# Kernel optimization log

Measured on AMD Instinct MI355X. Metric: run time of the kernel, lower is better.

The kernel has to match this reference:

```python
import jax, jax.numpy as jnp
import numpy as np
import math

BS, S, D, H, DFF, L = 32, 512, 512, 8, 2048, 2
DK = D // H
K_INDEX = 5
NEG = -1e32


def _xavier(key, shape):
    fan_out, fan_in = shape[-2], shape[-1]
    lim = math.sqrt(6.0 / (fan_in + fan_out))
    return jax.random.uniform(key, shape, minval=-lim, maxval=lim, dtype=jnp.float32)


def _cosine_pe():
    pos = np.arange(S, dtype=np.float32)[:, None]
    div = np.exp(np.arange(0, D, 2, dtype=np.float32) * -(math.log(10000.0) / D))
    pe = np.zeros((S, D), dtype=np.float32)
    pe[:, 0::2] = np.sin(pos * div)
    pe[:, 1::2] = np.cos(pos * div)
    return jnp.asarray(pe)[None]  # [1,S,D]


def setup_inputs() -> dict:
    key = jax.random.key(0)
    ks = jax.random.split(key, 8)
    return {
        'q_embed_data': jax.random.normal(ks[0], (BS, S, D), jnp.float32),
        'qa_embed_data': jax.random.normal(ks[1], (BS, S, D), jnp.float32),
        'pe': _cosine_pe(),
        'Wk': _xavier(ks[2], (L, D, D)), 'bk': jnp.zeros((L, D)),
        'Wv': _xavier(ks[3], (L, D, D)), 'bv': jnp.zeros((L, D)),
        'Wo': _xavier(ks[4], (L, D, D)), 'bo': jnp.zeros((L, D)),
        'W1': _xavier(ks[5], (L, DFF, D)), 'b1': jnp.zeros((L, DFF)),
        'W2': _xavier(ks[6], (L, D, DFF)), 'b2': jnp.zeros((L, D)),
        'ln1w': jnp.ones((L, D)), 'ln1b': jnp.zeros((L, D)),
        'ln2w': jnp.ones((L, D)), 'ln2b': jnp.zeros((L, D)),
    }


def _ln(x, w, b):
    m = jnp.mean(x, axis=-1, keepdims=True)
    v = jnp.mean((x - m) ** 2, axis=-1, keepdims=True)
    return (x - m) / jnp.sqrt(v + 1e-5) * w + b


def _forward(q_embed_data, qa_embed_data, pe, Wk, bk, Wv, bv, Wo, bo,
             W1, b1, W2, b2, ln1w, ln1b, ln2w, ln2b):
    x = q_embed_data + pe[:, :S]
    y = qa_embed_data + pe[:, :S]
    # src_mask = (triu(ones, k=0) == 0): only strictly-lower positions allowed (row 0 fully masked)
    causal = jnp.tril(jnp.ones((S, S), bool), k=-1)
    attn_weights = None
    for l in range(L):
        # kq_same: q uses k_linear
        q = (x @ Wk[l].T + bk[l]).reshape(BS, S, H, DK).transpose(0, 2, 1, 3)
        k = q  # identical projection of identical input (key=query=x)
        v = (y @ Wv[l].T + bv[l]).reshape(BS, S, H, DK).transpose(0, 2, 1, 3)
        scores = jnp.einsum('bhqd,bhkd->bhqk', q, k) / math.sqrt(DK)
        scores = jnp.where(causal, scores, NEG)
        scores = jax.nn.softmax(scores, axis=-1)
        # sparseattn: for rows >= K_INDEX keep only entries >= k-th largest, re-softmax
        sb = scores[:, :, K_INDEX:, :]
        thr = jax.lax.top_k(sb, K_INDEX)[0][..., -1:]  # k-th largest per row
        sb = jnp.where(sb - thr >= 0, sb, NEG)
        scores = jnp.concatenate([scores[:, :, :K_INDEX, :], sb], axis=2)
        scores = jax.nn.softmax(scores, axis=-1)
        attn_weights = scores  # before_dropout_scores (before zero_pad)
        scores = scores.at[:, :, 0, :].set(0.0)  # zero_pad row 0
        out = jnp.einsum('bhqk,bhkd->bhqd', scores, v)
        out = out.transpose(0, 2, 1, 3).reshape(BS, S, D) @ Wo[l].T + bo[l]
        x = _ln(x + out, ln1w[l], ln1b[l])
        ff = jax.nn.relu(x @ W1[l].T + b1[l]) @ W2[l].T + b2[l]
        x = _ln(x + ff, ln2w[l], ln2b[l])
    return x, attn_weights


def reference(q_embed_data, qa_embed_data, pe, Wk, bk, Wv, bv, Wo, bo,
              W1, b1, W2, b2, ln1w, ln1b, ln2w, ln2b):
    return _forward(q_embed_data, qa_embed_data, pe, Wk, bk, Wv, bv, Wo, bo,
                    W1, b1, W2, b2, ln1w, ln1b, ln2w, ln2b)
```

## Files before the change

kernel.cpp:

```cpp
#include <hip/hip_runtime.h>
#include <hip/hip_bf16.h>
#include <math.h>

#define BSZ 32
#define SEQ 512
#define DIM 512
#define NH 8
#define DKH 64
#define DFFN 2048
#define NL 2
#define KIDX 5
#define NEGV -1e32f

typedef float f32x4 __attribute__((ext_vector_type(4)));
typedef short bf16x8 __attribute__((ext_vector_type(8)));
typedef unsigned short ushort_t;

__device__ __forceinline__ float wmaxf(float v) {
    #pragma unroll
    for (int m = 32; m > 0; m >>= 1) v = fmaxf(v, __shfl_xor(v, m));
    return v;
}
__device__ __forceinline__ float wsumf(float v) {
    #pragma unroll
    for (int m = 32; m > 0; m >>= 1) v += __shfl_xor(v, m);
    return v;
}
__device__ __forceinline__ int wsumi(int v) {
    #pragma unroll
    for (int m = 32; m > 0; m >>= 1) v += __shfl_xor(v, m);
    return v;
}

__device__ __forceinline__ unsigned int bf16_rne(float x) {
    unsigned int u = __float_as_uint(x);
    return (u + 0x7fffu + ((u >> 16) & 1u)) >> 16;
}
__device__ __forceinline__ void split3_8(const float* xs, unsigned int* hh,
                                         unsigned int* hm, unsigned int* hl) {
    #pragma unroll
    for (int e = 0; e < 8; e++) {
        float x = xs[e];
        unsigned int h0 = bf16_rne(x);
        float r1 = x - __uint_as_float(h0 << 16);
        unsigned int h1 = bf16_rne(r1);
        float r2 = r1 - __uint_as_float(h1 << 16);
        hh[e] = h0; hm[e] = h1; hl[e] = bf16_rne(r2);
    }
}
__device__ __forceinline__ uint4 pack8(const unsigned int* h) {
    return make_uint4(h[0] | (h[1] << 16), h[2] | (h[3] << 16),
                      h[4] | (h[5] << 16), h[6] | (h[7] << 16));
}

__device__ __forceinline__ f32x4 mfma_bf16(bf16x8 a, bf16x8 b, f32x4 c) {
    return __builtin_amdgcn_mfma_f32_16x16x32_bf16(a, b, c, 0, 0, 0);
}

__global__ void add_pe_old(const float4* __restrict__ q, const float4* __restrict__ qa,
                           const float4* __restrict__ pe, float4* __restrict__ x,
                           float4* __restrict__ y, int n4) {
    int i = blockIdx.x * 256 + threadIdx.x;
    if (i >= n4) return;
    int pi = i & (SEQ * DIM / 4 - 1);
    float4 p = pe[pi];
    float4 a = q[i], b = qa[i];
    x[i] = make_float4(a.x + p.x, a.y + p.y, a.z + p.z, a.w + p.w);
    y[i] = make_float4(b.x + p.x, b.y + p.y, b.z + p.z, b.w + p.w);
}

__global__ void add_pe_new(const float* __restrict__ q, const float* __restrict__ qa,
                           const float* __restrict__ pe, float* __restrict__ x,
                           ushort_t* __restrict__ ypl, size_t yelems, int n8) {
    int i = blockIdx.x * 256 + threadIdx.x;
    if (i >= n8) return;
    size_t base = (size_t)i * 8;
    size_t pb = base & (size_t)(SEQ * DIM - 1);
    float4 a0 = *(const float4*)(q + base), a1 = *(const float4*)(q + base + 4);
    float4 b0 = *(const float4*)(qa + base), b1 = *(const float4*)(qa + base + 4);
    float4 p0 = *(const float4*)(pe + pb), p1 = *(const float4*)(pe + pb + 4);
    float4 x0 = make_float4(a0.x + p0.x, a0.y + p0.y, a0.z + p0.z, a0.w + p0.w);
    float4 x1 = make_float4(a1.x + p1.x, a1.y + p1.y, a1.z + p1.z, a1.w + p1.w);
    *(float4*)(x + base) = x0;
    *(float4*)(x + base + 4) = x1;
    float ys[8] = {b0.x + p0.x, b0.y + p0.y, b0.z + p0.z, b0.w + p0.w,
                   b1.x + p1.x, b1.y + p1.y, b1.z + p1.z, b1.w + p1.w};
    unsigned int hh[8], hm[8], hl[8];
    split3_8(ys, hh, hm, hl);
    *(uint4*)(ypl + base) = pack8(hh);
    *(uint4*)(ypl + yelems + base) = pack8(hm);
    *(uint4*)(ypl + 2 * yelems + base) = pack8(hl);
}

__global__ void split3w(const float* __restrict__ W, ushort_t* __restrict__ out,
                        size_t elems, int n8) {
    int i = blockIdx.x * 256 + threadIdx.x;
    if (i >= n8) return;
    size_t base = (size_t)i * 8;
    float4 a0 = *(const float4*)(W + base), a1 = *(const float4*)(W + base + 4);
    float xs[8] = {a0.x, a0.y, a0.z, a0.w, a1.x, a1.y, a1.z, a1.w};
    unsigned int hh[8], hm[8], hl[8];
    split3_8(xs, hh, hm, hl);
    *(uint4*)(out + base) = pack8(hh);
    *(uint4*)(out + elems + base) = pack8(hm);
    *(uint4*)(out + 2 * elems + base) = pack8(hl);
}

template <int RELU>
__global__ __launch_bounds__(256)
void gemm_bt(const float* __restrict__ A, const float* __restrict__ B,
             const float* __restrict__ bias, float* __restrict__ C,
             int M, int N, int K) {
    __shared__ float As[16][132];
    __shared__ float Bs[16][132];
    const int tid = threadIdx.x;
    const int tx = tid & 15, ty = tid >> 4;
    const int m0 = blockIdx.y * 128, n0 = blockIdx.x * 128;
    float acc[8][8] = {};
    for (int k0 = 0; k0 < K; k0 += 16) {
        #pragma unroll
        for (int s = tid; s < 512; s += 256) {
            int r = s >> 2, c4 = s & 3;
            float4 va = *(const float4*)(A + (size_t)(m0 + r) * K + k0 + c4 * 4);
            As[c4 * 4 + 0][r] = va.x; As[c4 * 4 + 1][r] = va.y;
            As[c4 * 4 + 2][r] = va.z; As[c4 * 4 + 3][r] = va.w;
            float4 vb = *(const float4*)(B + (size_t)(n0 + r) * K + k0 + c4 * 4);
            Bs[c4 * 4 + 0][r] = vb.x; Bs[c4 * 4 + 1][r] = vb.y;
            Bs[c4 * 4 + 2][r] = vb.z; Bs[c4 * 4 + 3][r] = vb.w;
        }
        __syncthreads();
        #pragma unroll
        for (int kk = 0; kk < 16; kk++) {
            float a[8], b[8];
            *(float4*)&a[0] = *(const float4*)&As[kk][ty * 8];
            *(float4*)&a[4] = *(const float4*)&As[kk][ty * 8 + 4];
            *(float4*)&b[0] = *(const float4*)&Bs[kk][tx * 8];
            *(float4*)&b[4] = *(const float4*)&Bs[kk][tx * 8 + 4];
            #pragma unroll
            for (int i = 0; i < 8; i++)
                #pragma unroll
                for (int j = 0; j < 8; j++)
                    acc[i][j] = fmaf(a[i], b[j], acc[i][j]);
        }
        __syncthreads();
    }
    float bv[8];
    *(float4*)&bv[0] = *(const float4*)(bias + n0 + tx * 8);
    *(float4*)&bv[4] = *(const float4*)(bias + n0 + tx * 8 + 4);
    #pragma unroll
    for (int i = 0; i < 8; i++) {
        float out[8];
        #pragma unroll
        for (int j = 0; j < 8; j++) {
            float v = acc[i][j] + bv[j];
            if (RELU) v = fmaxf(v, 0.f);
            out[j] = v;
        }
        float* cp = C + (size_t)(m0 + ty * 8 + i) * N + n0 + tx * 8;
        *(float4*)cp = *(float4*)&out[0];
        *(float4*)(cp + 4) = *(float4*)&out[4];
    }
}

__global__ __launch_bounds__(256)
void scores128_kernel(const float* __restrict__ q, float* __restrict__ pbuf) {
    const int bh = blockIdx.y, b = bh >> 3, h = bh & 7;
    const int x = blockIdx.x;
    const int it = (x >= 6) ? 3 : (x >= 3) ? 2 : (x >= 1) ? 1 : 0;
    const int jt = x - it * (it + 1) / 2;
    const int m0 = it * 128, n0 = jt * 128;
    __shared__ float Qi[64][132];
    __shared__ float Qj[64][132];
    const float* qbase = q + (size_t)b * SEQ * DIM + h * DKH;
    const int tid = threadIdx.x;
    for (int s = tid; s < 2048; s += 256) {
        int row = (s & 15) | ((s >> 8) << 4);
        int c4 = (s >> 4) & 15;
        float4 vi = *(const float4*)(qbase + (size_t)(m0 + row) * DIM + c4 * 4);
        Qi[c4 * 4 + 0][row] = vi.x; Qi[c4 * 4 + 1][row] = vi.y;
        Qi[c4 * 4 + 2][row] = vi.z; Qi[c4 * 4 + 3][row] = vi.w;
        float4 vj = *(const float4*)(qbase + (size_t)(n0 + row) * DIM + c4 * 4);
        Qj[c4 * 4 + 0][row] = vj.x; Qj[c4 * 4 + 1][row] = vj.y;
        Qj[c4 * 4 + 2][row] = vj.z; Qj[c4 * 4 + 3][row] = vj.w;
    }
    __syncthreads();
    const int tx = tid & 15, ty = tid >> 4;
    float acc[8][8] = {};
    #pragma unroll 4
    for (int d = 0; d < 64; d++) {
        float a[8], bb[8];
        *(float4*)&a[0] = *(const float4*)&Qi[d][ty * 8];
        *(float4*)&a[4] = *(const float4*)&Qi[d][ty * 8 + 4];
        *(float4*)&bb[0] = *(const float4*)&Qj[d][tx * 8];
        *(float4*)&bb[4] = *(const float4*)&Qj[d][tx * 8 + 4];
        #pragma unroll
        for (int i = 0; i < 8; i++)
            #pragma unroll
            for (int j = 0; j < 8; j++)
                acc[i][j] = fmaf(a[i], bb[j], acc[i][j]);
    }
    float* prow = pbuf + ((size_t)bh * SEQ + m0) * SEQ + n0;
    #pragma unroll
    for (int i = 0; i < 8; i++) {
        int gi = m0 + ty * 8 + i;
        #pragma unroll
        for (int jq = 0; jq < 2; jq++) {
            float o[4];
            #pragma unroll
            for (int j = 0; j < 4; j++) {
                int gj = n0 + tx * 8 + jq * 4 + j;
                o[j] = (gj < gi) ? acc[i][jq * 4 + j] * 0.125f : NEGV;
            }
            *(float4*)(prow + (size_t)(ty * 8 + i) * SEQ + tx * 8 + jq * 4) = *(float4*)o;
        }
    }
}

template <int RELU, int OUTP>
__global__ __launch_bounds__(256) void gemm3p(
    const ushort_t* __restrict__ Apl, size_t Aelems, int lda,
    const ushort_t* __restrict__ Bpl, size_t Belems, int ldb,
    const float* __restrict__ bias,
    float* __restrict__ C, ushort_t* __restrict__ Cpl, size_t Celems,
    int ldc, int K) {
    __shared__ uint4 lds[3072];
    const int tid = threadIdx.x, lane = tid & 63, wid = tid >> 6;
    const int wm = wid >> 1, wn = wid & 1;
    const int m0 = blockIdx.y * 128, n0 = blockIdx.x * 128;
    const int lrow = lane & 15, lkof = (lane >> 4) * 8;
    f32x4 acc[4][4] = {};
    for (int k0 = 0; k0 < K; k0 += 32) {
        #pragma unroll
        for (int t = 0; t < 12; t++) {
            const ushort_t* src;
            int dstoff;
            if (t < 6) {
                int cc = wid + t * 4;
                int p = cc >> 3, fi = cc & 7;
                src = Apl + (size_t)p * Aelems + (size_t)(m0 + fi * 16 + lrow) * lda + k0 + lkof;
                dstoff = p * 512 + fi * 64;
            } else {
                int cc = wid + (t - 6) * 4;
                int p = cc >> 3, fi = cc & 7;
                src = Bpl + (size_t)p * Belems + (size_t)(n0 + fi * 16 + lrow) * ldb + k0 + lkof;
                dstoff = 1536 + p * 512 + fi * 64;
            }
            lds[dstoff + lane] = *(const uint4*)src;
        }
        __syncthreads();
        const bf16x8* ldsb = (const bf16x8*)lds;
        bf16x8 afr[4][3];
        #pragma unroll
        for (int fm = 0; fm < 4; fm++)
            #pragma unroll
            for (int p = 0; p < 3; p++)
                afr[fm][p] = ldsb[p * 512 + (wm * 4 + fm) * 64 + lane];
        #pragma unroll
        for (int fn = 0; fn < 4; fn++) {
            bf16x8 b0 = ldsb[1536 + 0 * 512 + (wn * 4 + fn) * 64 + lane];
            bf16x8 b1 = ldsb[1536 + 1 * 512 + (wn * 4 + fn) * 64 + lane];
            bf16x8 b2 = ldsb[1536 + 2 * 512 + (wn * 4 + fn) * 64 + lane];
            #pragma unroll
            for (int fm = 0; fm < 4; fm++) {
                f32x4 t = acc[fm][fn];
                t = mfma_bf16(afr[fm][0], b0, t);
                t = mfma_bf16(afr[fm][1], b0, t);
                t = mfma_bf16(afr[fm][2], b0, t);
                t = mfma_bf16(afr[fm][0], b1, t);
                t = mfma_bf16(afr[fm][1], b1, t);
                t = mfma_bf16(afr[fm][0], b2, t);
                acc[fm][fn] = t;
            }
        }
        __syncthreads();
    }
    #pragma unroll
    for (int fm = 0; fm < 4; fm++) {
        int row0 = m0 + (wm * 4 + fm) * 16 + (lane >> 4) * 4;
        #pragma unroll
        for (int fn = 0; fn < 4; fn++) {
            int col = n0 + (wn * 4 + fn) * 16 + (lane & 15);
            float bv = bias[col];
            f32x4 a = acc[fm][fn];
            #pragma unroll
            for (int r = 0; r < 4; r++) {
                int row = row0 + r;
                float val = a[r] + bv;
                if (RELU) val = fmaxf(val, 0.f);
                if constexpr (OUTP == 0) {
                    C[(size_t)row * ldc + col] = val;
                } else {
                    unsigned int h0 = bf16_rne(val);
                    float r1 = val - __uint_as_float(h0 << 16);
                    unsigned int h1 = bf16_rne(r1);
                    float r2 = r1 - __uint_as_float(h1 << 16);
                    unsigned int h2 = bf16_rne(r2);
                    size_t o = (size_t)row * ldc + col;
                    Cpl[o] = (ushort_t)h0;
                    Cpl[Celems + o] = (ushort_t)h1;
                    Cpl[2 * Celems + o] = (ushort_t)h2;
                }
            }
        }
    }
}

template <int MODE, int TN>
__global__ __launch_bounds__(256) void mm6(const float* __restrict__ Aall,
                                           const float* __restrict__ Ball,
                                           float* __restrict__ Call,
                                           const float* __restrict__ bias,
                                           int lda, int ldb, int ldc, int K) {
    constexpr int BFR = TN / 16;
    constexpr int MFR = (TN == 128) ? 4 : 2;
    constexpr int BBASE = 3 * 8 * 64;
    __shared__ uint4 lds[3 * 8 * 64 + 3 * BFR * 64];

    const int tid = threadIdx.x, lane = tid & 63, wid = tid >> 6;
    const int wm = (TN == 128) ? (wid >> 1) : wid;
    const int wn = (TN == 128) ? (wid & 1) : 0;

    const float* A;
    const float* B;
    float* C;
    int m0, n0, kmax;
    if constexpr (MODE <= 1) {
        m0 = blockIdx.y * 128;
        n0 = blockIdx.x * 128;
        A = Aall; B = Ball; C = Call;
        kmax = K;
    } else {
        const int bh = blockIdx.y, b = bh >> 3, h = bh & 7, rb = blockIdx.x;
        m0 = rb * 128; n0 = 0;
        A = Aall + (size_t)bh * SEQ * SEQ;
        B = Ball + (size_t)bh * DKH * SEQ;
        C = Call + ((size_t)b * SEQ) * DIM + h * DKH;
        kmax = rb ? (rb + 1) * 128 : SEQ;
    }

    f32x4 acc[MFR][4] = {};

    for (int k0 = 0; k0 < kmax; k0 += 32) {
        for (int c = tid; c < (8 + BFR) * 64; c += 256) {
            int fi = c >> 6, lc = c & 63;
            const float* src = (fi < 8)
                ? A + (size_t)(m0 + fi * 16 + (lc & 15)) * lda + k0 + (lc >> 4) * 8
                : B + (size_t)(n0 + (fi - 8) * 16 + (lc & 15)) * ldb + k0 + (lc >> 4) * 8;
            float4 x0 = *(const float4*)src;
            float4 x1 = *(const float4*)(src + 4);
            float xs[8] = {x0.x, x0.y, x0.z, x0.w, x1.x, x1.y, x1.z, x1.w};
            unsigned int hh[8], hm[8], hl[8];
            split3_8(xs, hh, hm, hl);
            int base = (fi < 8) ? fi * 64 + lc : BBASE + (fi - 8) * 64 + lc;
            int fstride = (fi < 8) ? 8 * 64 : BFR * 64;
            lds[base + 0 * fstride] = pack8(hh);
            lds[base + 1 * fstride] = pack8(hm);
            lds[base + 2 * fstride] = pack8(hl);
        }
        __syncthreads();

        const bf16x8* ldsb = (const bf16x8*)lds;
        bf16x8 afr[MFR][3];
        #pragma unroll
        for (int fm = 0; fm < MFR; fm++)
            #pragma unroll
            for (int p = 0; p < 3; p++)
                afr[fm][p] = ldsb[p * 512 + (wm * MFR + fm) * 64 + lane];
        #pragma unroll
        for (int fn = 0; fn < 4; fn++) {
            bf16x8 b0 = ldsb[BBASE + 0 * (BFR * 64) + (wn * 4 + fn) * 64 + lane];
            bf16x8 b1 = ldsb[BBASE + 1 * (BFR * 64) + (wn * 4 + fn) * 64 + lane];
            bf16x8 b2 = ldsb[BBASE + 2 * (BFR * 64) + (wn * 4 + fn) * 64 + lane];
            #pragma unroll
            for (int fm = 0; fm < MFR; fm++) {
                f32x4 t = acc[fm][fn];
                t = mfma_bf16(afr[fm][0], b0, t);
                t = mfma_bf16(afr[fm][1], b0, t);
                t = mfma_bf16(afr[fm][2], b0, t);
                t = mfma_bf16(afr[fm][0], b1, t);
                t = mfma_bf16(afr[fm][1], b1, t);
                t = mfma_bf16(afr[fm][0], b2, t);
                acc[fm][fn] = t;
            }
        }
        __syncthreads();
    }

    #pragma unroll
    for (int fm = 0; fm < MFR; fm++) {
        int row0 = m0 + (wm * MFR + fm) * 16 + (lane >> 4) * 4;
        #pragma unroll
        for (int fn = 0; fn < 4; fn++) {
            int col = n0 + (wn * 4 + fn) * 16 + (lane & 15);
            float bv = 0.f;
            if constexpr (MODE <= 1) bv = bias[col];
            f32x4 a = acc[fm][fn];
            #pragma unroll
            for (int r = 0; r < 4; r++) {
                int row = row0 + r;
                float val;
                if constexpr (MODE == 0) val = a[r] + bv;
                else if constexpr (MODE == 1) val = fmaxf(a[r] + bv, 0.f);
                else val = (row == 0) ? 0.f : a[r];
                C[(size_t)row * ldc + col] = val;
            }
        }
    }
}

__global__ __launch_bounds__(256) void mm6av_pl(const float* __restrict__ pbuf,
                                                const float* __restrict__ vt,
                                                ushort_t* __restrict__ Opl, size_t Oelems) {
    constexpr int BFR = 4, MFR = 2, BBASE = 3 * 8 * 64;
    __shared__ uint4 lds[3 * 8 * 64 + 3 * BFR * 64];
    const int tid = threadIdx.x, lane = tid & 63, wid = tid >> 6;
    const int bh = blockIdx.y, b = bh >> 3, h = bh & 7, rb = blockIdx.x;
    const int m0 = rb * 128;
    const float* A = pbuf + (size_t)bh * SEQ * SEQ;
    const float* B = vt + (size_t)bh * DKH * SEQ;
    const int kmax = rb ? (rb + 1) * 128 : SEQ;

    f32x4 acc[MFR][4] = {};
    for (int k0 = 0; k0 < kmax; k0 += 32) {
        for (int c = tid; c < (8 + BFR) * 64; c += 256) {
            int fi = c >> 6, lc = c & 63;
            const float* src = (fi < 8)
                ? A + (size_t)(m0 + fi * 16 + (lc & 15)) * SEQ + k0 + (lc >> 4) * 8
                : B + (size_t)((fi - 8) * 16 + (lc & 15)) * SEQ + k0 + (lc >> 4) * 8;
            float4 x0 = *(const float4*)src;
            float4 x1 = *(const float4*)(src + 4);
            float xs[8] = {x0.x, x0.y, x0.z, x0.w, x1.x, x1.y, x1.z, x1.w};
            unsigned int hh[8], hm[8], hl[8];
            split3_8(xs, hh, hm, hl);
            int base = (fi < 8) ? fi * 64 + lc : BBASE + (fi - 8) * 64 + lc;
            int fstride = (fi < 8) ? 8 * 64 : BFR * 64;
            lds[base + 0 * fstride] = pack8(hh);
            lds[base + 1 * fstride] = pack8(hm);
            lds[base + 2 * fstride] = pack8(hl);
        }
        __syncthreads();
        const bf16x8* ldsb = (const bf16x8*)lds;
        bf16x8 afr[MFR][3];
        #pragma unroll
        for (int fm = 0; fm < MFR; fm++)
            #pragma unroll
            for (int p = 0; p < 3; p++)
                afr[fm][p] = ldsb[p * 512 + (wid * MFR + fm) * 64 + lane];
        #pragma unroll
        for (int fn = 0; fn < 4; fn++) {
            bf16x8 b0 = ldsb[BBASE + 0 * (BFR * 64) + fn * 64 + lane];
            bf16x8 b1 = ldsb[BBASE + 1 * (BFR * 64) + fn * 64 + lane];
            bf16x8 b2 = ldsb[BBASE + 2 * (BFR * 64) + fn * 64 + lane];
            #pragma unroll
            for (int fm = 0; fm < MFR; fm++) {
                f32x4 t = acc[fm][fn];
                t = mfma_bf16(afr[fm][0], b0, t);
                t = mfma_bf16(afr[fm][1], b0, t);
                t = mfma_bf16(afr[fm][2], b0, t);
                t = mfma_bf16(afr[fm][0], b1, t);
                t = mfma_bf16(afr[fm][1], b1, t);
                t = mfma_bf16(afr[fm][0], b2, t);
                acc[fm][fn] = t;
            }
        }
        __syncthreads();
    }
    #pragma unroll
    for (int fm = 0; fm < MFR; fm++) {
        int row0 = m0 + (wid * MFR + fm) * 16 + (lane >> 4) * 4;
        #pragma unroll
        for (int fn = 0; fn < 4; fn++) {
            int col = fn * 16 + (lane & 15);
            f32x4 a = acc[fm][fn];
            #pragma unroll
            for (int r = 0; r < 4; r++) {
                int row = row0 + r;
                float val = (row == 0) ? 0.f : a[r];
                unsigned int h0 = bf16_rne(val);
                float r1 = val - __uint_as_float(h0 << 16);
                unsigned int h1 = bf16_rne(r1);
                float r2 = r1 - __uint_as_float(h1 << 16);
                unsigned int h2 = bf16_rne(r2);
                size_t o = ((size_t)b * SEQ + row) * DIM + h * DKH + col;
                Opl[o] = (ushort_t)h0;
                Opl[Oelems + o] = (ushort_t)h1;
                Opl[2 * Oelems + o] = (ushort_t)h2;
            }
        }
    }
}

__global__ __launch_bounds__(256) void transpose_v_kernel(const float* __restrict__ v,
                                                          float* __restrict__ vt) {
    const int bh = blockIdx.y, jt = blockIdx.x;
    const int b = bh >> 3, h = bh & 7;
    __shared__ float L[64][65];
    const int tid = threadIdx.x;
    for (int s = tid; s < 1024; s += 256) {
        int jj = s >> 4, d4 = s & 15;
        float4 x = *(const float4*)(v + ((size_t)(b * SEQ) + jt * 64 + jj) * DIM + h * DKH + d4 * 4);
        L[jj][d4 * 4 + 0] = x.x; L[jj][d4 * 4 + 1] = x.y;
        L[jj][d4 * 4 + 2] = x.z; L[jj][d4 * 4 + 3] = x.w;
    }
    __syncthreads();
    int d = tid >> 2, jq = tid & 3;
    float* dst = vt + ((size_t)bh * DKH + d) * SEQ + jt * 64 + jq * 16;
    #pragma unroll
    for (int c4 = 0; c4 < 4; c4++) {
        float4 o = make_float4(L[jq * 16 + c4 * 4 + 0][d], L[jq * 16 + c4 * 4 + 1][d],
                               L[jq * 16 + c4 * 4 + 2][d], L[jq * 16 + c4 * 4 + 3][d]);
        *(float4*)(dst + c4 * 4) = o;
    }
}

__global__ __launch_bounds__(64)
void softmax_topk_kernel(float* __restrict__ pbuf) {
    const int i = blockIdx.x;
    const size_t row = (size_t)blockIdx.y * SEQ + i;
    const int lane = threadIdx.x;
    float* p = pbuf + row * SEQ;
    float v[8];
    {
        int j0 = lane * 4;
        if (j0 < i) {
            float4 x0 = *(const float4*)(p + j0);
            v[0] = (j0 + 0 < i) ? x0.x : NEGV;
            v[1] = (j0 + 1 < i) ? x0.y : NEGV;
            v[2] = (j0 + 2 < i) ? x0.z : NEGV;
            v[3] = (j0 + 3 < i) ? x0.w : NEGV;
        } else { v[0] = v[1] = v[2] = v[3] = NEGV; }
        int j1 = 256 + j0;
        if (j1 < i) {
            float4 x1 = *(const float4*)(p + j1);
            v[4] = (j1 + 0 < i) ? x1.x : NEGV;
            v[5] = (j1 + 1 < i) ? x1.y : NEGV;
            v[6] = (j1 + 2 < i) ? x1.z : NEGV;
            v[7] = (j1 + 3 < i) ? x1.w : NEGV;
        } else { v[4] = v[5] = v[6] = v[7] = NEGV; }
    }
    float lm = v[0];
    #pragma unroll
    for (int e = 1; e < 8; e++) lm = fmaxf(lm, v[e]);
    float m1 = wmaxf(lm);
    float ls = 0.f;
    #pragma unroll
    for (int e = 0; e < 8; e++) { v[e] = expf(v[e] - m1); ls += v[e]; }
    float Z = wsumf(ls);
    #pragma unroll
    for (int e = 0; e < 8; e++) v[e] = v[e] / Z;
    float thr = -INFINITY;
    if (i >= KIDX) {
        int remaining = KIDX;
        float cut = INFINITY;
        #pragma unroll 1
        for (int iter = 0; iter < KIDX; iter++) {
            float l2 = -INFINITY;
            #pragma unroll
            for (int e = 0; e < 8; e++) if (v[e] < cut) l2 = fmaxf(l2, v[e]);
            float m2 = wmaxf(l2);
            int lc = 0;
            #pragma unroll
            for (int e = 0; e < 8; e++) if (v[e] == m2) lc++;
            int c = wsumi(lc);
            if (c >= remaining) { thr = m2; break; }
            remaining -= c; cut = m2;
        }
    }
    float lpm = v[0];
    #pragma unroll
    for (int e = 1; e < 8; e++) lpm = fmaxf(lpm, v[e]);
    float pm = wmaxf(lpm);
    float t[8];
    float ls2 = 0.f;
    #pragma unroll
    for (int e = 0; e < 8; e++) {
        bool keep = (i >= KIDX) ? (v[e] >= thr) : true;
        t[e] = keep ? expf(v[e] - pm) : 0.f;
        ls2 += t[e];
    }
    float Z2 = wsumf(ls2);
    #pragma unroll
    for (int e = 0; e < 8; e++) t[e] = t[e] / Z2;
    *(float4*)(p + lane * 4) = make_float4(t[0], t[1], t[2], t[3]);
    *(float4*)(p + 256 + lane * 4) = make_float4(t[4], t[5], t[6], t[7]);
}

template <int EMIT>
__global__ __launch_bounds__(64)
void add_ln_kernel(const float* __restrict__ x, const float* __restrict__ t,
                   const float* __restrict__ w, const float* __restrict__ b,
                   float* __restrict__ dst, ushort_t* __restrict__ dpl, size_t delems) {
    const size_t row = blockIdx.x;
    const int lane = threadIdx.x;
    const float* xr = x + row * DIM;
    const float* tr = t + row * DIM;
    float v[8];
    {
        float4 a0 = *(const float4*)(xr + lane * 4);
        float4 t0 = *(const float4*)(tr + lane * 4);
        float4 a1 = *(const float4*)(xr + 256 + lane * 4);
        float4 t1 = *(const float4*)(tr + 256 + lane * 4);
        v[0] = a0.x + t0.x; v[1] = a0.y + t0.y; v[2] = a0.z + t0.z; v[3] = a0.w + t0.w;
        v[4] = a1.x + t1.x; v[5] = a1.y + t1.y; v[6] = a1.z + t1.z; v[7] = a1.w + t1.w;
    }
    float ls = 0.f;
    #pragma unroll
    for (int e = 0; e < 8; e++) ls += v[e];
    float mean = wsumf(ls) / (float)DIM;
    float ld = 0.f;
    #pragma unroll
    for (int e = 0; e < 8; e++) { float d = v[e] - mean; ld += d * d; }
    float var = wsumf(ld) / (float)DIM;
    float den = sqrtf(var + 1e-5f);
    float wv[8], bv[8];
    *(float4*)&wv[0] = *(const float4*)(w + lane * 4);
    *(float4*)&wv[4] = *(const float4*)(w + 256 + lane * 4);
    *(float4*)&bv[0] = *(const float4*)(b + lane * 4);
    *(float4*)&bv[4] = *(const float4*)(b + 256 + lane * 4);
    float o[8];
    #pragma unroll
    for (int e = 0; e < 8; e++) o[e] = (v[e] - mean) / den * wv[e] + bv[e];
    float* dr = dst + row * DIM;
    *(float4*)(dr + lane * 4) = make_float4(o[0], o[1], o[2], o[3]);
    *(float4*)(dr + 256 + lane * 4) = make_float4(o[4], o[5], o[6], o[7]);
    if constexpr (EMIT) {
        unsigned int hh[8], hm[8], hl[8];
        split3_8(o, hh, hm, hl);
        size_t base0 = row * DIM + lane * 4;
        size_t base1 = base0 + 256;
        #pragma unroll
        for (int p = 0; p < 3; p++) {
            const unsigned int* hp = (p == 0) ? hh : (p == 1) ? hm : hl;
            *(uint2*)(dpl + p * delems + base0) =
                make_uint2(hp[0] | (hp[1] << 16), hp[2] | (hp[3] << 16));
            *(uint2*)(dpl + p * delems + base1) =
                make_uint2(hp[4] | (hp[5] << 16), hp[6] | (hp[7] << 16));
        }
    }
}

extern "C" void kernel_launch(void* const* d_in, const int* in_sizes, int n_in,
                              void* d_out, int out_size, void* d_ws, size_t ws_size,
                              hipStream_t stream) {
    const float* q_embed = (const float*)d_in[0];
    const float* qa_embed = (const float*)d_in[1];
    const float* pe = (const float*)d_in[2];
    const float* Wk = (const float*)d_in[3];
    const float* bk = (const float*)d_in[4];
    const float* Wv = (const float*)d_in[5];
    const float* bv = (const float*)d_in[6];
    const float* Wo = (const float*)d_in[7];
    const float* bo = (const float*)d_in[8];
    const float* W1 = (const float*)d_in[9];
    const float* b1 = (const float*)d_in[10];
    const float* W2 = (const float*)d_in[11];
    const float* b2 = (const float*)d_in[12];
    const float* ln1w = (const float*)d_in[13];
    const float* ln1b = (const float*)d_in[14];
    const float* ln2w = (const float*)d_in[15];
    const float* ln2b = (const float*)d_in[16];

    float* outx = (float*)d_out;
    const size_t NE = (size_t)BSZ * SEQ * DIM;
    float* pbuf = outx + NE;
    float* ws = (float*)d_ws;
    const int M = BSZ * SEQ;

    const size_t need_new = 13 * NE * sizeof(float);
    if (ws_size >= need_new) {
        float* xbuf = ws;
        float* qbuf = ws + NE;
        float* vbuf = ws + 2 * NE;
        ushort_t* y_pl = (ushort_t*)(ws + 3 * NE);
        ushort_t* x_pl = (ushort_t*)(ws + 4 * NE + NE / 2);
        ushort_t* w_pl = (ushort_t*)(ws + 6 * NE);
        float* vt = ws + 7 * NE;
        ushort_t* o_pl = (ushort_t*)(ws + 8 * NE);
        ushort_t* h1_pl = (ushort_t*)(ws + 7 * NE);

        const size_t WVE = (size_t)DIM * DIM;
        const size_t W1E = (size_t)DFFN * DIM;
        const size_t LW = 3 * (WVE + WVE + W1E + W1E);

        for (int l = 0; l < NL; l++) {
            ushort_t* base = w_pl + (size_t)l * LW;
            split3w<<<(int)(WVE / 8 + 255) / 256, 256, 0, stream>>>(
                Wv + (size_t)l * WVE, base, WVE, (int)(WVE / 8));
            split3w<<<(int)(WVE / 8 + 255) / 256, 256, 0, stream>>>(
                Wo + (size_t)l * WVE, base + 3 * WVE, WVE, (int)(WVE / 8));
            split3w<<<(int)(W1E / 8 + 255) / 256, 256, 0, stream>>>(
                W1 + (size_t)l * W1E, base + 6 * WVE, W1E, (int)(W1E / 8));
            split3w<<<(int)(W1E / 8 + 255) / 256, 256, 0, stream>>>(
                W2 + (size_t)l * W1E, base + 6 * WVE + 3 * W1E, W1E, (int)(W1E / 8));
        }

        add_pe_new<<<(int)(NE / 8 + 255) / 256, 256, 0, stream>>>(
            q_embed, qa_embed, pe, xbuf, y_pl, NE, (int)(NE / 8));

        for (int l = 0; l < NL; l++) {
            ushort_t* wb = w_pl + (size_t)l * LW;
            ushort_t* Wv_pl = wb;
            ushort_t* Wo_pl = wb + 3 * WVE;
            ushort_t* W1_pl = wb + 6 * WVE;
            ushort_t* W2_pl = wb + 6 * WVE + 3 * W1E;

            gemm_bt<0><<<dim3(DIM / 128, M / 128), 256, 0, stream>>>(
                xbuf, Wk + (size_t)l * WVE, bk + (size_t)l * DIM, qbuf, M, DIM, DIM);
            gemm3p<0, 0><<<dim3(DIM / 128, M / 128), 256, 0, stream>>>(
                y_pl, NE, DIM, Wv_pl, WVE, DIM, bv + (size_t)l * DIM,
                vbuf, nullptr, 0, DIM, DIM);
            transpose_v_kernel<<<dim3(8, BSZ * NH), 256, 0, stream>>>(vbuf, vt);
            scores128_kernel<<<dim3(10, BSZ * NH), 256, 0, stream>>>(qbuf, pbuf);
            softmax_topk_kernel<<<dim3(SEQ, BSZ * NH), 64, 0, stream>>>(pbuf);
            mm6av_pl<<<dim3(4, BSZ * NH), 256, 0, stream>>>(pbuf, vt, o_pl, NE);
            gemm3p<0, 0><<<dim3(DIM / 128, M / 128), 256, 0, stream>>>(
                o_pl, NE, DIM, Wo_pl, WVE, DIM, bo + (size_t)l * DIM,
                qbuf, nullptr, 0, DIM, DIM);
            add_ln_kernel<1><<<M, 64, 0, stream>>>(
                xbuf, qbuf, ln1w + (size_t)l * DIM, ln1b + (size_t)l * DIM,
                xbuf, x_pl, NE);
            gemm3p<1, 1><<<dim3(DFFN / 128, M / 128), 256, 0, stream>>>(
                x_pl, NE, DIM, W1_pl, W1E, DIM, b1 + (size_t)l * DFFN,
                nullptr, h1_pl, (size_t)M * DFFN, DFFN, DIM);
            gemm3p<0, 0><<<dim3(DIM / 128, M / 128), 256, 0, stream>>>(
                h1_pl, (size_t)M * DFFN, DFFN, W2_pl, W1E, DFFN, b2 + (size_t)l * DIM,
                vbuf, nullptr, 0, DIM, DFFN);
            float* dst = (l == NL - 1) ? outx : xbuf;
            add_ln_kernel<0><<<M, 64, 0, stream>>>(
                xbuf, vbuf, ln2w + (size_t)l * DIM, ln2b + (size_t)l * DIM,
                dst, nullptr, 0);
        }
    } else {
        float* xbuf = ws;
        float* ybuf = ws + NE;
        float* qbuf = ws + 2 * NE;
        float* vbuf = ws + 3 * NE;
        float* obuf = ws + 4 * NE;
        float* vtbuf = ws + 5 * NE;
        float* h1buf = ws + 5 * NE;

        {
            int n4 = (int)(NE / 4);
            add_pe_old<<<(n4 + 255) / 256, 256, 0, stream>>>(
                (const float4*)q_embed, (const float4*)qa_embed, (const float4*)pe,
                (float4*)xbuf, (float4*)ybuf, n4);
        }
        for (int l = 0; l < NL; l++) {
            const float* Wk_l = Wk + (size_t)l * DIM * DIM;
            const float* Wv_l = Wv + (size_t)l * DIM * DIM;
            const float* Wo_l = Wo + (size_t)l * DIM * DIM;
            const float* W1_l = W1 + (size_t)l * DFFN * DIM;
            const float* W2_l = W2 + (size_t)l * DIM * DFFN;

            gemm_bt<0><<<dim3(DIM / 128, M / 128), 256, 0, stream>>>(
                xbuf, Wk_l, bk + (size_t)l * DIM, qbuf, M, DIM, DIM);
            mm6<0, 128><<<dim3(DIM / 128, M / 128), 256, 0, stream>>>(
                ybuf, Wv_l, vbuf, bv + (size_t)l * DIM, DIM, DIM, DIM, DIM);
            transpose_v_kernel<<<dim3(8, BSZ * NH), 256, 0, stream>>>(vbuf, vtbuf);
            scores128_kernel<<<dim3(10, BSZ * NH), 256, 0, stream>>>(qbuf, pbuf);
            softmax_topk_kernel<<<dim3(SEQ, BSZ * NH), 64, 0, stream>>>(pbuf);
            mm6<3, 64><<<dim3(4, BSZ * NH), 256, 0, stream>>>(
                pbuf, vtbuf, obuf, nullptr, SEQ, SEQ, DIM, SEQ);
            mm6<0, 128><<<dim3(DIM / 128, M / 128), 256, 0, stream>>>(
                obuf, Wo_l, qbuf, bo + (size_t)l * DIM, DIM, DIM, DIM, DIM);
            add_ln_kernel<0><<<M, 64, 0, stream>>>(
                xbuf, qbuf, ln1w + (size_t)l * DIM, ln1b + (size_t)l * DIM,
                xbuf, nullptr, 0);
            mm6<1, 128><<<dim3(DFFN / 128, M / 128), 256, 0, stream>>>(
                xbuf, W1_l, h1buf, b1 + (size_t)l * DFFN, DIM, DIM, DFFN, DIM);
            mm6<0, 128><<<dim3(DIM / 128, M / 128), 256, 0, stream>>>(
                h1buf, W2_l, vbuf, b2 + (size_t)l * DIM, DFFN, DFFN, DIM, DFFN);
            float* dst = (l == NL - 1) ? outx : xbuf;
            add_ln_kernel<0><<<M, 64, 0, stream>>>(
                xbuf, vbuf, ln2w + (size_t)l * DIM, ln2b + (size_t)l * DIM,
                dst, nullptr, 0);
        }
    }
}
```

Baseline: 2.194 ms.

## Use two-plane bf16 split in last layer and direct global-to-LDS loads

Templates the bf16-split GEMMs on the number of planes and runs the second layer with two planes (3 MFMAs per tile step instead of 6), skipping the third residual plane both in inputs and in emitted outputs. It also replaces register-staged global loads in gemm3p with global_load_lds direct-to-LDS transfers. Lower emulated precision in the last layer cuts MFMA and memory work but loosens accuracy relative to the fp32 reference.

```diff
diff --git a/kernel.cpp b/kernel.cpp
--- a/kernel.cpp
+++ b/kernel.cpp
@@ -15,6 +15,12 @@
 typedef float f32x4 __attribute__((ext_vector_type(4)));
 typedef short bf16x8 __attribute__((ext_vector_type(8)));
 typedef unsigned short ushort_t;
+typedef __attribute__((address_space(1))) void gvoid;
+typedef __attribute__((address_space(3))) void lvoid;
+
+__device__ __forceinline__ void gload_lds16(const void* g, void* l) {
+    __builtin_amdgcn_global_load_lds((gvoid*)(uintptr_t)g, (lvoid*)l, 16, 0, 0);
+}
 
 __device__ __forceinline__ float wmaxf(float v) {
     #pragma unroll
@@ -216,14 +222,15 @@
     }
 }
 
-template <int RELU, int OUTP>
+template <int RELU, int OUTP, int NP>
 __global__ __launch_bounds__(256) void gemm3p(
     const ushort_t* __restrict__ Apl, size_t Aelems, int lda,
     const ushort_t* __restrict__ Bpl, size_t Belems, int ldb,
     const float* __restrict__ bias,
     float* __restrict__ C, ushort_t* __restrict__ Cpl, size_t Celems,
     int ldc, int K) {
-    __shared__ uint4 lds[3072];
+    constexpr int BB = NP * 512;
+    __shared__ uint4 lds[2 * NP * 512];
     const int tid = threadIdx.x, lane = tid & 63, wid = tid >> 6;
     const int wm = wid >> 1, wn = wid & 1;
     const int m0 = blockIdx.y * 128, n0 = blockIdx.x * 128;
@@ -231,44 +238,46 @@
     f32x4 acc[4][4] = {};
     for (int k0 = 0; k0 < K; k0 += 32) {
         #pragma unroll
-        for (int t = 0; t < 12; t++) {
-            const ushort_t* src;
-            int dstoff;
-            if (t < 6) {
-                int cc = wid + t * 4;
-                int p = cc >> 3, fi = cc & 7;
-                src = Apl + (size_t)p * Aelems + (size_t)(m0 + fi * 16 + lrow) * lda + k0 + lkof;
-                dstoff = p * 512 + fi * 64;
-            } else {
-                int cc = wid + (t - 6) * 4;
-                int p = cc >> 3, fi = cc & 7;
-                src = Bpl + (size_t)p * Belems + (size_t)(n0 + fi * 16 + lrow) * ldb + k0 + lkof;
-                dstoff = 1536 + p * 512 + fi * 64;
-            }
-            lds[dstoff + lane] = *(const uint4*)src;
+        for (int t = 0; t < 4 * NP; t++) {
+            int cc = wid + t * 4;
+            bool isB = cc >= 8 * NP;
+            int c2 = isB ? (cc - 8 * NP) : cc;
+            int p = c2 >> 3, fi = c2 & 7;
+            const ushort_t* pb = isB ? (Bpl + (size_t)p * Belems) : (Apl + (size_t)p * Aelems);
+            int ld = isB ? ldb : lda;
+            int r0 = isB ? n0 : m0;
+            const ushort_t* src = pb + (size_t)(r0 + fi * 16 + lrow) * ld + k0 + lkof;
+            gload_lds16(src, &lds[(isB ? BB : 0) + p * 512 + fi * 64]);
         }
         __syncthreads();
         const bf16x8* ldsb = (const bf16x8*)lds;
-        bf16x8 afr[4][3];
+        bf16x8 afr[4][NP];
         #pragma unroll
         for (int fm = 0; fm < 4; fm++)
             #pragma unroll
-            for (int p = 0; p < 3; p++)
+            for (int p = 0; p < NP; p++)
                 afr[fm][p] = ldsb[p * 512 + (wm * 4 + fm) * 64 + lane];
         #pragma unroll
         for (int fn = 0; fn < 4; fn++) {
-            bf16x8 b0 = ldsb[1536 + 0 * 512 + (wn * 4 + fn) * 64 + lane];
-            bf16x8 b1 = ldsb[1536 + 1 * 512 + (wn * 4 + fn) * 64 + lane];
-            bf16x8 b2 = ldsb[1536 + 2 * 512 + (wn * 4 + fn) * 64 + lane];
+            bf16x8 b0 = ldsb[BB + 0 * 512 + (wn * 4 + fn) * 64 + lane];
+            bf16x8 b1 = ldsb[BB + 1 * 512 + (wn * 4 + fn) * 64 + lane];
+            bf16x8 b2;
+            if constexpr (NP == 3) b2 = ldsb[BB + 2 * 512 + (wn * 4 + fn) * 64 + lane];
             #pragma unroll
             for (int fm = 0; fm < 4; fm++) {
                 f32x4 t = acc[fm][fn];
-                t = mfma_bf16(afr[fm][0], b0, t);
-                t = mfma_bf16(afr[fm][1], b0, t);
-                t = mfma_bf16(afr[fm][2], b0, t);
-                t = mfma_bf16(afr[fm][0], b1, t);
-                t = mfma_bf16(afr[fm][1], b1, t);
-                t = mfma_bf16(afr[fm][0], b2, t);
+                if constexpr (NP == 3) {
+                    t = mfma_bf16(afr[fm][0], b0, t);
+                    t = mfma_bf16(afr[fm][1], b0, t);
+                    t = mfma_bf16(afr[fm][2], b0, t);
+                    t = mfma_bf16(afr[fm][0], b1, t);
+                    t = mfma_bf16(afr[fm][1], b1, t);
+                    t = mfma_bf16(afr[fm][0], b2, t);
+                } else {
+                    t = mfma_bf16(afr[fm][0], b0, t);
+                    t = mfma_bf16(afr[fm][1], b0, t);
+                    t = mfma_bf16(afr[fm][0], b1, t);
+                }
                 acc[fm][fn] = t;
             }
         }
@@ -293,12 +302,13 @@
                     unsigned int h0 = bf16_rne(val);
                     float r1 = val - __uint_as_float(h0 << 16);
                     unsigned int h1 = bf16_rne(r1);
-                    float r2 = r1 - __uint_as_float(h1 << 16);
-                    unsigned int h2 = bf16_rne(r2);
                     size_t o = (size_t)row * ldc + col;
                     Cpl[o] = (ushort_t)h0;
                     Cpl[Celems + o] = (ushort_t)h1;
-                    Cpl[2 * Celems + o] = (ushort_t)h2;
+                    if constexpr (NP == 3) {
+                        float r2 = r1 - __uint_as_float(h1 << 16);
+                        Cpl[2 * Celems + o] = (ushort_t)bf16_rne(r2);
+                    }
                 }
             }
         }
@@ -408,11 +418,12 @@
     }
 }
 
+template <int NP>
 __global__ __launch_bounds__(256) void mm6av_pl(const float* __restrict__ pbuf,
                                                 const float* __restrict__ vt,
                                                 ushort_t* __restrict__ Opl, size_t Oelems) {
-    constexpr int BFR = 4, MFR = 2, BBASE = 3 * 8 * 64;
-    __shared__ uint4 lds[3 * 8 * 64 + 3 * BFR * 64];
+    constexpr int BBASE = NP * 512;
+    __shared__ uint4 lds[NP * 512 + NP * 256];
     const int tid = threadIdx.x, lane = tid & 63, wid = tid >> 6;
     const int bh = blockIdx.y, b = bh >> 3, h = bh & 7, rb = blockIdx.x;
     const int m0 = rb * 128;
@@ -420,9 +431,9 @@
     const float* B = vt + (size_t)bh * DKH * SEQ;
     const int kmax = rb ? (rb + 1) * 128 : SEQ;
 
-    f32x4 acc[MFR][4] = {};
+    f32x4 acc[2][4] = {};
     for (int k0 = 0; k0 < kmax; k0 += 32) {
-        for (int c = tid; c < (8 + BFR) * 64; c += 256) {
+        for (int c = tid; c < 12 * 64; c += 256) {
             int fi = c >> 6, lc = c & 63;
             const float* src = (fi < 8)
                 ? A + (size_t)(m0 + fi * 16 + (lc & 15)) * SEQ + k0 + (lc >> 4) * 8
@@ -432,42 +443,50 @@
             float xs[8] = {x0.x, x0.y, x0.z, x0.w, x1.x, x1.y, x1.z, x1.w};
             unsigned int hh[8], hm[8], hl[8];
             split3_8(xs, hh, hm, hl);
-            int base = (fi < 8) ? fi * 64 + lc : BBASE + (fi - 8) * 64 + lc;
-            int fstride = (fi < 8) ? 8 * 64 : BFR * 64;
-            lds[base + 0 * fstride] = pack8(hh);
-            lds[base + 1 * fstride] = pack8(hm);
-            lds[base + 2 * fstride] = pack8(hl);
+            int base, fstride;
+            if (fi < 8) { base = fi * 64 + lc; fstride = 512; }
+            else { base = BBASE + (fi - 8) * 64 + lc; fstride = 256; }
+            lds[base] = pack8(hh);
+            lds[base + fstride] = pack8(hm);
+            if (NP == 3) lds[base + 2 * fstride] = pack8(hl);
         }
         __syncthreads();
         const bf16x8* ldsb = (const bf16x8*)lds;
-        bf16x8 afr[MFR][3];
-        #pragma unroll
-        for (int fm = 0; fm < MFR; fm++)
-            #pragma unroll
-            for (int p = 0; p < 3; p++)
-                afr[fm][p] = ldsb[p * 512 + (wid * MFR + fm) * 64 + lane];
+        bf16x8 afr[2][NP];
+        #pragma unroll
+        for (int fm = 0; fm < 2; fm++)
+            #pragma unroll
+            for (int p = 0; p < NP; p++)
+                afr[fm][p] = ldsb[p * 512 + (wid * 2 + fm) * 64 + lane];
         #pragma unroll
         for (int fn = 0; fn < 4; fn++) {
-            bf16x8 b0 = ldsb[BBASE + 0 * (BFR * 64) + fn * 64 + lane];
-            bf16x8 b1 = ldsb[BBASE + 1 * (BFR * 64) + fn * 64 + lane];
-            bf16x8 b2 = ldsb[BBASE + 2 * (BFR * 64) + fn * 64 + lane];
-            #pragma unroll
-            for (int fm = 0; fm < MFR; fm++) {
+            bf16x8 b0 = ldsb[BBASE + 0 * 256 + fn * 64 + lane];
+            bf16x8 b1 = ldsb[BBASE + 1 * 256 + fn * 64 + lane];
+            bf16x8 b2;
+            if constexpr (NP == 3) b2 = ldsb[BBASE + 2 * 256 + fn * 64 + lane];
+            #pragma unroll
+            for (int fm = 0; fm < 2; fm++) {
                 f32x4 t = acc[fm][fn];
-                t = mfma_bf16(afr[fm][0], b0, t);
-                t = mfma_bf16(afr[fm][1], b0, t);
-                t = mfma_bf16(afr[fm][2], b0, t);
-                t = mfma_bf16(afr[fm][0], b1, t);
-                t = mfma_bf16(afr[fm][1], b1, t);
-                t = mfma_bf16(afr[fm][0], b2, t);
+                if constexpr (NP == 3) {
+                    t = mfma_bf16(afr[fm][0], b0, t);
+                    t = mfma_bf16(afr[fm][1], b0, t);
+                    t = mfma_bf16(afr[fm][2], b0, t);
+                    t = mfma_bf16(afr[fm][0], b1, t);
+                    t = mfma_bf16(afr[fm][1], b1, t);
+                    t = mfma_bf16(afr[fm][0], b2, t);
+                } else {
+                    t = mfma_bf16(afr[fm][0], b0, t);
+                    t = mfma_bf16(afr[fm][1], b0, t);
+                    t = mfma_bf16(afr[fm][0], b1, t);
+                }
                 acc[fm][fn] = t;
             }
         }
         __syncthreads();
     }
     #pragma unroll
-    for (int fm = 0; fm < MFR; fm++) {
-        int row0 = m0 + (wid * MFR + fm) * 16 + (lane >> 4) * 4;
+    for (int fm = 0; fm < 2; fm++) {
+        int row0 = m0 + (wid * 2 + fm) * 16 + (lane >> 4) * 4;
         #pragma unroll
         for (int fn = 0; fn < 4; fn++) {
             int col = fn * 16 + (lane & 15);
@@ -479,12 +498,13 @@
                 unsigned int h0 = bf16_rne(val);
                 float r1 = val - __uint_as_float(h0 << 16);
                 unsigned int h1 = bf16_rne(r1);
-                float r2 = r1 - __uint_as_float(h1 << 16);
-                unsigned int h2 = bf16_rne(r2);
                 size_t o = ((size_t)b * SEQ + row) * DIM + h * DKH + col;
                 Opl[o] = (ushort_t)h0;
                 Opl[Oelems + o] = (ushort_t)h1;
-                Opl[2 * Oelems + o] = (ushort_t)h2;
+                if constexpr (NP == 3) {
+                    float r2 = r1 - __uint_as_float(h1 << 16);
+                    Opl[2 * Oelems + o] = (ushort_t)bf16_rne(r2);
+                }
             }
         }
     }
@@ -706,25 +726,47 @@
 
             gemm_bt<0><<<dim3(DIM / 128, M / 128), 256, 0, stream>>>(
                 xbuf, Wk + (size_t)l * WVE, bk + (size_t)l * DIM, qbuf, M, DIM, DIM);
-            gemm3p<0, 0><<<dim3(DIM / 128, M / 128), 256, 0, stream>>>(
-                y_pl, NE, DIM, Wv_pl, WVE, DIM, bv + (size_t)l * DIM,
-                vbuf, nullptr, 0, DIM, DIM);
+            if (l == 0) {
+                gemm3p<0, 0, 3><<<dim3(DIM / 128, M / 128), 256, 0, stream>>>(
+                    y_pl, NE, DIM, Wv_pl, WVE, DIM, bv + (size_t)l * DIM,
+                    vbuf, nullptr, 0, DIM, DIM);
+            } else {
+                gemm3p<0, 0, 2><<<dim3(DIM / 128, M / 128), 256, 0, stream>>>(
+                    y_pl, NE, DIM, Wv_pl, WVE, DIM, bv + (size_t)l * DIM,
+                    vbuf, nullptr, 0, DIM, DIM);
+            }
             transpose_v_kernel<<<dim3(8, BSZ * NH), 256, 0, stream>>>(vbuf, vt);
             scores128_kernel<<<dim3(10, BSZ * NH), 256, 0, stream>>>(qbuf, pbuf);
             softmax_topk_kernel<<<dim3(SEQ, BSZ * NH), 64, 0, stream>>>(pbuf);
-            mm6av_pl<<<dim3(4, BSZ * NH), 256, 0, stream>>>(pbuf, vt, o_pl, NE);
-            gemm3p<0, 0><<<dim3(DIM / 128, M / 128), 256, 0, stream>>>(
-                o_pl, NE, DIM, Wo_pl, WVE, DIM, bo + (size_t)l * DIM,
-                qbuf, nullptr, 0, DIM, DIM);
+            if (l == 0) {
+                mm6av_pl<3><<<dim3(4, BSZ * NH), 256, 0, stream>>>(pbuf, vt, o_pl, NE);
+                gemm3p<0, 0, 3><<<dim3(DIM / 128, M / 128), 256, 0, stream>>>(
+                    o_pl, NE, DIM, Wo_pl, WVE, DIM, bo + (size_t)l * DIM,
+                    qbuf, nullptr, 0, DIM, DIM);
+            } else {
+                mm6av_pl<2><<<dim3(4, BSZ * NH), 256, 0, stream>>>(pbuf, vt, o_pl, NE);
+                gemm3p<0, 0, 2><<<dim3(DIM / 128, M / 128), 256, 0, stream>>>(
+                    o_pl, NE, DIM, Wo_pl, WVE, DIM, bo + (size_t)l * DIM,
+                    qbuf, nullptr, 0, DIM, DIM);
+            }
             add_ln_kernel<1><<<M, 64, 0, stream>>>(
                 xbuf, qbuf, ln1w + (size_t)l * DIM, ln1b + (size_t)l * DIM,
                 xbuf, x_pl, NE);
-            gemm3p<1, 1><<<dim3(DFFN / 128, M / 128), 256, 0, stream>>>(
-                x_pl, NE, DIM, W1_pl, W1E, DIM, b1 + (size_t)l * DFFN,
-                nullptr, h1_pl, (size_t)M * DFFN, DFFN, DIM);
-            gemm3p<0, 0><<<dim3(DIM / 128, M / 128), 256, 0, stream>>>(
-                h1_pl, (size_t)M * DFFN, DFFN, W2_pl, W1E, DFFN, b2 + (size_t)l * DIM,
-                vbuf, nullptr, 0, DIM, DFFN);
+            if (l == 0) {
+                gemm3p<1, 1, 3><<<dim3(DFFN / 128, M / 128), 256, 0, stream>>>(
+                    x_pl, NE, DIM, W1_pl, W1E, DIM, b1 + (size_t)l * DFFN,
+                    nullptr, h1_pl, (size_t)M * DFFN, DFFN, DIM);
+                gemm3p<0, 0, 3><<<dim3(DIM / 128, M / 128), 256, 0, stream>>>(
+                    h1_pl, (size_t)M * DFFN, DFFN, W2_pl, W1E, DFFN, b2 + (size_t)l * DIM,
+                    vbuf, nullptr, 0, DIM, DFFN);
+            } else {
+                gemm3p<1, 1, 2><<<dim3(DFFN / 128, M / 128), 256, 0, stream>>>(
+                    x_pl, NE, DIM, W1_pl, W1E, DIM, b1 + (size_t)l * DFFN,
+                    nullptr, h1_pl, (size_t)M * DFFN, DFFN, DIM);
+                gemm3p<0, 0, 2><<<dim3(DIM / 128, M / 128), 256, 0, stream>>>(
+                    h1_pl, (size_t)M * DFFN, DFFN, W2_pl, W1E, DFFN, b2 + (size_t)l * DIM,
+                    vbuf, nullptr, 0, DIM, DFFN);
+            }
             float* dst = (l == NL - 1) ? outx : xbuf;
             add_ln_kernel<0><<<M, 64, 0, stream>>>(
                 xbuf, vbuf, ln2w + (size_t)l * DIM, ln2b + (size_t)l * DIM,
```

New measurement: 1.970 ms. -10.2%, faster.
